# Kernel tuning notes

Hardware: AMD Instinct MI355X
Metric: run time of the kernel (lower is better)

Reference implementation:

```python
import jax, jax.numpy as jnp
import numpy as np

CHUNK = 32  # chunk_size default in delta_rule_chunkwise


def _l2norm(x):
    # matches fla-style l2norm: x / ||x||_2 along last dim
    return x * jax.lax.rsqrt(jnp.sum(x * x, axis=-1, keepdims=True) + 1e-6)


def setup_inputs() -> dict:
    key = jax.random.key(0)
    kq, kk, kv, kb = jax.random.split(key, 4)
    b, h, L, dk, dv = 4, 8, 8192, 64, 64
    q = jax.random.normal(kq, (b, h, L, dk), jnp.float32)
    k = jax.random.normal(kk, (b, h, L, dk), jnp.float32)
    v = jax.random.normal(kv, (b, h, L, dv), jnp.float32)
    beta = jax.random.uniform(kb, (b, h, L), jnp.float32)  # sigmoid(b_proj) in (0,1)
    return {"q": q, "k": k, "v": v, "beta": beta}


def _delta_rule_chunkwise(q, k, v, beta, chunk=CHUNK):
    b, h, L, dk = q.shape
    dv = v.shape[-1]
    assert L % chunk == 0  # L chosen as multiple of chunk -> pad_len == 0
    n = L // chunk

    q = _l2norm(q)
    k = _l2norm(k)
    v = v * beta[..., None]
    k_beta = k * beta[..., None]

    # (b,h,L,d) -> (b,h,n,c,d)
    resh = lambda t: t.reshape(b, h, n, chunk, t.shape[-1])
    qc, kc, vc, kbc = resh(q), resh(k), resh(v), resh(k_beta)

    # intra-chunk triangular inversion: attn = (I - tril(k_beta k^T, -1))^{-1}
    tri = jnp.triu(jnp.ones((chunk, chunk), bool), 0)  # incl. diagonal
    attn = -jnp.einsum('bhnid,bhnjd->bhnij', kbc, kc)
    attn = jnp.where(tri, 0.0, attn)
    for i in range(1, chunk):  # static forward-substitution loop over chunk rows
        row = attn[..., i, :]                                  # (b,h,n,c)
        upd = jnp.einsum('bhnj,bhnjm->bhnm', row, attn)[..., :i]
        attn = attn.at[..., i, :i].add(upd)
    attn = attn + jnp.eye(chunk, dtype=attn.dtype)

    u = attn @ vc   # (b,h,n,c,dv)
    w = attn @ kbc  # (b,h,n,c,dk)

    strict = jnp.triu(jnp.ones((chunk, chunk), bool), 1)

    def step(S, xs):
        q_i, k_i, u_i0, w_i = xs  # (b,h,c,d)
        attn_local = jnp.where(strict, 0.0,
                               jnp.einsum('bhid,bhjd->bhij', q_i, k_i))
        u_i = u_i0 - w_i @ S                       # (b,h,c,dv)
        o_i = q_i @ S + attn_local @ u_i           # (b,h,c,dv)
        S_new = S + jnp.einsum('bhcd,bhcv->bhdv', k_i, u_i)
        return S_new, o_i

    to_scan = lambda t: jnp.moveaxis(t, 2, 0)  # (n,b,h,c,d)
    S0 = jnp.zeros((b, h, dk, dv), q.dtype)
    S, o = jax.lax.scan(step, S0, (to_scan(qc), to_scan(kc), to_scan(u), to_scan(w)))
    o = jnp.moveaxis(o, 0, 2).reshape(b, h, L, dv)
    return o, S


def reference(q, k, v, beta):
    return _delta_rule_chunkwise(q, k, v, beta)
```

## Files before the change

kernel.cpp:

```cpp
#include <hip/hip_runtime.h>

#define CH 32
#define DD 64
#define NCHUNK 256
#define SEQ 8192
#define BH 32
#define NSEG 16
#define CPS 16

typedef _Float16 half8 __attribute__((ext_vector_type(8)));
typedef float f32x4 __attribute__((ext_vector_type(4)));
typedef unsigned short u16;

#define MFMA16(a, b, c) __builtin_amdgcn_mfma_f32_16x16x32_f16((a), (b), (c), 0, 0, 0)

__device__ __forceinline__ void split_store(const float* src8, bool neg, u16* dst) {
    half8 hi, lo;
#pragma unroll
    for (int j = 0; j < 8; ++j) {
        float x = neg ? -src8[j] : src8[j];
        _Float16 xh = (_Float16)x;
        hi[j] = xh;
        lo[j] = (_Float16)(x - (float)xh);
    }
    *(half8*)dst = hi;
    *(half8*)(dst + 8) = lo;
}

__device__ __forceinline__ void hi_store(const float* src8, u16* dst) {
    half8 hi;
#pragma unroll
    for (int j = 0; j < 8; ++j) hi[j] = (_Float16)src8[j];
    *(half8*)dst = hi;
}

__device__ __forceinline__ void split8(const float* src8, half8* hi, half8* lo) {
#pragma unroll
    for (int j = 0; j < 8; ++j) {
        float x = src8[j];
        _Float16 xh = (_Float16)x;
        (*hi)[j] = xh;
        (*lo)[j] = (_Float16)(x - (float)xh);
    }
}

__device__ __forceinline__ void splitB(const f32x4& a, const f32x4& b, half8* hi, half8* lo) {
#pragma unroll
    for (int j = 0; j < 4; ++j) {
        float x = a[j];
        _Float16 xh = (_Float16)x;
        (*hi)[j] = xh; (*lo)[j] = (_Float16)(x - (float)xh);
    }
#pragma unroll
    for (int j = 0; j < 4; ++j) {
        float x = b[j];
        _Float16 xh = (_Float16)x;
        (*hi)[4 + j] = xh; (*lo)[4 + j] = (_Float16)(x - (float)xh);
    }
}

__global__ __launch_bounds__(256) void prep_kernel(
    float* __restrict__ q, float* __restrict__ k,
    const float* __restrict__ v, const float* __restrict__ beta,
    float* __restrict__ u_out, u16* __restrict__ qfrag, u16* __restrict__ pfrag)
{
    const int blk = blockIdx.x;
    const int bh = blk >> 8;
    const int cc = blk & 255;
    const size_t base = ((size_t)bh * SEQ + (size_t)cc * CH) * DD;
    const int t = threadIdx.x;

    __shared__ __align__(16) float qs[CH][68];
    __shared__ __align__(16) float ks[CH][68];
    __shared__ __align__(16) float kb[CH][68];
    __shared__ __align__(16) float vb[CH][68];
    __shared__ __align__(16) float wl[CH][68];
    __shared__ float A[CH][33];
    __shared__ __align__(16) float Pl[CH][36];
    __shared__ float bet[CH];
    __shared__ float rnq[CH];
    __shared__ float rnk[CH];

    if (t < CH) bet[t] = beta[(size_t)bh * SEQ + (size_t)cc * CH + t];
    for (int rep = 0; rep < 2; ++rep) {
        int idx = t + rep * 256;
        int r = idx >> 4, d4 = idx & 15;
        float4 vq = *(const float4*)&q[base + (size_t)idx * 4];
        float4 vk = *(const float4*)&k[base + (size_t)idx * 4];
        float4 vv = *(const float4*)&v[base + (size_t)idx * 4];
        *(float4*)&qs[r][4 * d4] = vq;
        *(float4*)&ks[r][4 * d4] = vk;
        *(float4*)&vb[r][4 * d4] = vv;
    }
    __syncthreads();
    if (t < CH) {
        float ss = 0.f;
        for (int d4 = 0; d4 < 16; ++d4) {
            float4 x = *(const float4*)&qs[t][4 * d4];
            ss += x.x * x.x + x.y * x.y + x.z * x.z + x.w * x.w;
        }
        rnq[t] = rsqrtf(ss + 1e-6f);
    } else if (t < 2 * CH) {
        int r = t - CH;
        float ss = 0.f;
        for (int d4 = 0; d4 < 16; ++d4) {
            float4 x = *(const float4*)&ks[r][4 * d4];
            ss += x.x * x.x + x.y * x.y + x.z * x.z + x.w * x.w;
        }
        rnk[r] = rsqrtf(ss + 1e-6f);
    }
    __syncthreads();
    for (int rep = 0; rep < 2; ++rep) {
        int idx = t + rep * 256;
        int r = idx >> 4, d4 = idx & 15;
        float4 vq = *(const float4*)&qs[r][4 * d4];
        float4 vk = *(const float4*)&ks[r][4 * d4];
        float4 vv = *(const float4*)&vb[r][4 * d4];
        float fq = rnq[r], fk = rnk[r], fb = bet[r];
        vq.x *= fq; vq.y *= fq; vq.z *= fq; vq.w *= fq;
        vk.x *= fk; vk.y *= fk; vk.z *= fk; vk.w *= fk;
        float4 vkb = make_float4(vk.x * fb, vk.y * fb, vk.z * fb, vk.w * fb);
        float4 vvb = make_float4(vv.x * fb, vv.y * fb, vv.z * fb, vv.w * fb);
        *(float4*)&qs[r][4 * d4] = vq;
        *(float4*)&ks[r][4 * d4] = vk;
        *(float4*)&kb[r][4 * d4] = vkb;
        *(float4*)&vb[r][4 * d4] = vvb;
    }
    __syncthreads();
    {
        const int l = t & 63, n = l & 15, h = l >> 4;
        const int wv = t >> 6, mt = wv >> 1, nt = wv & 1;
        half8 kbhi[2], kblo[2], qhi[2], qlo[2], khi[2], klo[2];
#pragma unroll
        for (int kt = 0; kt < 2; ++kt) {
            float a8[8], q8[8], b8[8];
#pragma unroll
            for (int jj = 0; jj < 8; ++jj) {
                a8[jj] = kb[16 * mt + n][32 * kt + 8 * h + jj];
                q8[jj] = qs[16 * mt + n][32 * kt + 8 * h + jj];
                b8[jj] = ks[16 * nt + n][32 * kt + 8 * h + jj];
            }
            split8(a8, &kbhi[kt], &kblo[kt]);
            split8(q8, &qhi[kt], &qlo[kt]);
            split8(b8, &khi[kt], &klo[kt]);
        }
        f32x4 gacc = {0.f, 0.f, 0.f, 0.f};
        f32x4 pacc = {0.f, 0.f, 0.f, 0.f};
#pragma unroll
        for (int kt = 0; kt < 2; ++kt) {
            gacc = MFMA16(kbhi[kt], khi[kt], gacc);
            gacc = MFMA16(kbhi[kt], klo[kt], gacc);
            gacc = MFMA16(kblo[kt], khi[kt], gacc);
            pacc = MFMA16(qhi[kt], khi[kt], pacc);
            pacc = MFMA16(qhi[kt], klo[kt], pacc);
            pacc = MFMA16(qlo[kt], khi[kt], pacc);
        }
#pragma unroll
        for (int i = 0; i < 4; ++i) {
            int ig = 16 * mt + 4 * h + i, jg = 16 * nt + n;
            A[ig][jg] = (jg < ig) ? -gacc[i] : 0.f;
            Pl[ig][jg] = (jg <= ig) ? pacc[i] : 0.f;
        }
    }
    __syncthreads();
    if (t < 64) {
        const int col = t & 31;
        float creg[CH];
        #pragma unroll
        for (int j = 0; j < CH; ++j) creg[j] = A[j][col];
        #pragma unroll
        for (int i = 1; i < CH; ++i) {
            float s = 0.f;
            #pragma unroll
            for (int j = 1; j < i; ++j) s += A[i][j] * creg[j];
            if (col < i) creg[i] += s;
        }
        if (t < 32) {
            #pragma unroll
            for (int j = 0; j < CH; ++j) A[j][col] = creg[j];
        }
    }
    __syncthreads();
    if (t < 128) {
        const int d4 = t & 15;
        const int i0 = (t >> 4) * 4;
        float4 su[4], sw[4];
        #pragma unroll
        for (int ii = 0; ii < 4; ++ii) {
            su[ii] = *(const float4*)&vb[i0 + ii][4 * d4];
            sw[ii] = *(const float4*)&kb[i0 + ii][4 * d4];
        }
        for (int j = 0; j <= i0 + 2; ++j) {
            float4 vv = *(const float4*)&vb[j][4 * d4];
            float4 vk = *(const float4*)&kb[j][4 * d4];
            #pragma unroll
            for (int ii = 0; ii < 4; ++ii) {
                float a = (j < i0 + ii) ? A[i0 + ii][j] : 0.f;
                su[ii].x += a * vv.x; su[ii].y += a * vv.y;
                su[ii].z += a * vv.z; su[ii].w += a * vv.w;
                sw[ii].x += a * vk.x; sw[ii].y += a * vk.y;
                sw[ii].z += a * vk.z; sw[ii].w += a * vk.w;
            }
        }
        #pragma unroll
        for (int ii = 0; ii < 4; ++ii) {
            *(float4*)&u_out[base + (size_t)(i0 + ii) * DD + 4 * d4] = su[ii];
            *(float4*)&wl[i0 + ii][4 * d4] = sw[ii];
        }
    }
    __syncthreads();
    {
        const int l = t & 63;
        const int n = l & 15, h = l >> 4;
        const int tw = t >> 6;
        const int mt = tw >> 1, kt = tw & 1;
        const size_t cslot = (size_t)bh * 256 + cc;
        {
            float tmp[8];
            #pragma unroll
            for (int j = 0; j < 8; ++j) tmp[j] = wl[mt * 16 + n][kt * 32 + h * 8 + j];
            split_store(tmp, true, (u16*)q + cslot * 4096 + (size_t)tw * 1024 + l * 16);
        }
        {
            float tmp[8];
            #pragma unroll
            for (int j = 0; j < 8; ++j) tmp[j] = ks[h * 8 + j][tw * 16 + n];
            split_store(tmp, false, (u16*)k + cslot * 4096 + (size_t)tw * 1024 + l * 16);
        }
        {
            float tmp[8];
            #pragma unroll
            for (int j = 0; j < 8; ++j) tmp[j] = qs[mt * 16 + n][kt * 32 + h * 8 + j];
            hi_store(tmp, qfrag + cslot * 2048 + (size_t)tw * 512 + l * 8);
        }
        if (t < 128) {
            float tmp[8];
            #pragma unroll
            for (int j = 0; j < 8; ++j) tmp[j] = Pl[tw * 16 + n][h * 8 + j];
            hi_store(tmp, pfrag + cslot * 1024 + (size_t)tw * 512 + l * 8);
        }
    }
}

__global__ __launch_bounds__(512) void seg_tf_kernel(
    const u16* __restrict__ wfrag, const u16* __restrict__ ktfrag,
    const float* __restrict__ uo, float* __restrict__ Tbuf, float* __restrict__ Bbuf)
{
    const int bhseg = blockIdx.x;
    const int bh = bhseg >> 4, seg = bhseg & (NSEG - 1);
    const int wv = threadIdx.x >> 6;
    const int g = wv & 3;
    const int tb = wv >> 2;
    const int l = threadIdx.x & 63;
    const int n = l & 15, h = l >> 4;
    const int c0 = seg * CPS, c1 = c0 + CPS;

    __shared__ __align__(16) float Sc[8][16 * 76];
    __shared__ __align__(16) float uc[8][16 * 44];

    const u16* wb = wfrag + (size_t)bh * 256 * 4096;
    const u16* kb = ktfrag + (size_t)bh * 256 * 4096;
    const float* ub = uo + (size_t)bh * SEQ * DD + (size_t)g * 16;

    f32x4 Sacc[4];
    const f32x4 fzero = {0.f, 0.f, 0.f, 0.f};
#pragma unroll
    for (int mt = 0; mt < 4; ++mt) Sacc[mt] = fzero;
    if (!tb) {
#pragma unroll
        for (int mt = 0; mt < 4; ++mt)
#pragma unroll
            for (int i = 0; i < 4; ++i)
                if (16 * mt + 4 * h + i == g * 16 + n) Sacc[mt][i] = 1.f;
    }

    half8 wcur[8];
    float u0cur[8];
#pragma unroll
    for (int z = 0; z < 8; ++z) u0cur[z] = 0.f;
    {
        const u16* wc = wb + (size_t)c0 * 4096;
#pragma unroll
        for (int tw = 0; tw < 4; ++tw) {
            wcur[tw * 2 + 0] = *(const half8*)(wc + (size_t)tw * 1024 + l * 16);
            wcur[tw * 2 + 1] = *(const half8*)(wc + (size_t)tw * 1024 + l * 16 + 8);
        }
        if (tb) {
#pragma unroll
            for (int mt = 0; mt < 2; ++mt)
#pragma unroll
                for (int i = 0; i < 4; ++i)
                    u0cur[mt * 4 + i] = ub[(size_t)(c0 * 32 + mt * 16 + h * 4 + i) * 64 + n];
        }
    }

    for (int c = c0; c < c1; ++c) {
        __syncthreads();
#pragma unroll
        for (int mt = 0; mt < 4; ++mt)
            *(f32x4*)&Sc[wv][n * 76 + mt * 16 + h * 4] = Sacc[mt];

        const u16* kc = kb + (size_t)c * 4096;
        half8 kT[8];
#pragma unroll
        for (int mt = 0; mt < 4; ++mt) {
            kT[mt * 2 + 0] = *(const half8*)(kc + (size_t)mt * 1024 + l * 16);
            kT[mt * 2 + 1] = *(const half8*)(kc + (size_t)mt * 1024 + l * 16 + 8);
        }

        const int cn = (c + 1 < c1) ? c + 1 : c;
        half8 wn[8];
        float u0n[8];
#pragma unroll
        for (int z = 0; z < 8; ++z) u0n[z] = 0.f;
        {
            const u16* wc = wb + (size_t)cn * 4096;
#pragma unroll
            for (int tw = 0; tw < 4; ++tw) {
                wn[tw * 2 + 0] = *(const half8*)(wc + (size_t)tw * 1024 + l * 16);
                wn[tw * 2 + 1] = *(const half8*)(wc + (size_t)tw * 1024 + l * 16 + 8);
            }
            if (tb) {
#pragma unroll
                for (int mt = 0; mt < 2; ++mt)
#pragma unroll
                    for (int i = 0; i < 4; ++i)
                        u0n[mt * 4 + i] = ub[(size_t)(cn * 32 + mt * 16 + h * 4 + i) * 64 + n];
            }
        }

        asm volatile("s_waitcnt lgkmcnt(0)" ::: "memory");
        half8 SBhi[2], SBlo[2];
#pragma unroll
        for (int kt = 0; kt < 2; ++kt) {
            f32x4 a = *(const f32x4*)&Sc[wv][n * 76 + kt * 32 + h * 8];
            f32x4 b = *(const f32x4*)&Sc[wv][n * 76 + kt * 32 + h * 8 + 4];
            splitB(a, b, &SBhi[kt], &SBlo[kt]);
        }

        f32x4 accu[2];
#pragma unroll
        for (int mt = 0; mt < 2; ++mt) {
            f32x4 a;
            a[0] = u0cur[mt * 4 + 0]; a[1] = u0cur[mt * 4 + 1];
            a[2] = u0cur[mt * 4 + 2]; a[3] = u0cur[mt * 4 + 3];
#pragma unroll
            for (int kt = 0; kt < 2; ++kt) {
                const int tw = mt * 2 + kt;
                a = MFMA16(wcur[tw * 2 + 0], SBhi[kt], a);
                a = MFMA16(wcur[tw * 2 + 0], SBlo[kt], a);
                a = MFMA16(wcur[tw * 2 + 1], SBhi[kt], a);
            }
            accu[mt] = a;
        }

#pragma unroll
        for (int mt = 0; mt < 2; ++mt)
            *(f32x4*)&uc[wv][n * 44 + mt * 16 + h * 4] = accu[mt];
        asm volatile("s_waitcnt lgkmcnt(0)" ::: "memory");
        half8 uBhi, uBlo;
        {
            f32x4 a = *(const f32x4*)&uc[wv][n * 44 + h * 8];
            f32x4 b = *(const f32x4*)&uc[wv][n * 44 + h * 8 + 4];
            splitB(a, b, &uBhi, &uBlo);
        }

#pragma unroll
        for (int mt = 0; mt < 4; ++mt) {
            f32x4 a = Sacc[mt];
            a = MFMA16(kT[mt * 2 + 0], uBhi, a);
            a = MFMA16(kT[mt * 2 + 0], uBlo, a);
            a = MFMA16(kT[mt * 2 + 1], uBhi, a);
            Sacc[mt] = a;
        }

#pragma unroll
        for (int z = 0; z < 8; ++z) wcur[z] = wn[z];
#pragma unroll
        for (int z = 0; z < 8; ++z) u0cur[z] = u0n[z];
    }

    float* ob = (tb ? Bbuf : Tbuf) + (size_t)bhseg * 4096;
#pragma unroll
    for (int mt = 0; mt < 4; ++mt)
#pragma unroll
        for (int i = 0; i < 4; ++i)
            ob[(size_t)(16 * mt + 4 * h + i) * 64 + g * 16 + n] = Sacc[mt][i];
}

__global__ __launch_bounds__(64) void compose_kernel(
    const float* __restrict__ Tbuf, const float* __restrict__ Bbuf,
    float* __restrict__ Sst, float* __restrict__ s_out)
{
    const int bh = blockIdx.x & 31;
    const int g = blockIdx.x >> 5;
    const int l = threadIdx.x;
    const int n = l & 15, h = l >> 4;
    __shared__ __align__(16) float Sc[16 * 76];

    f32x4 S[4];
    const f32x4 fzero = {0.f, 0.f, 0.f, 0.f};
#pragma unroll
    for (int mt = 0; mt < 4; ++mt) S[mt] = fzero;

    for (int s = 0; s < NSEG; ++s) {
        const size_t mb = (size_t)(bh * NSEG + s) * 4096;
#pragma unroll
        for (int mt = 0; mt < 4; ++mt)
#pragma unroll
            for (int i = 0; i < 4; ++i)
                Sst[mb + (size_t)(16 * mt + 4 * h + i) * 64 + g * 16 + n] = S[mt][i];

        f32x4 tr[16];
#pragma unroll
        for (int mt = 0; mt < 4; ++mt)
#pragma unroll
            for (int kkt = 0; kkt < 2; ++kkt) {
                tr[mt * 4 + kkt * 2 + 0] =
                    *(const f32x4*)&Tbuf[mb + (size_t)(16 * mt + n) * 64 + 32 * kkt + 8 * h];
                tr[mt * 4 + kkt * 2 + 1] =
                    *(const f32x4*)&Tbuf[mb + (size_t)(16 * mt + n) * 64 + 32 * kkt + 8 * h + 4];
            }
        f32x4 acc[4];
#pragma unroll
        for (int mt = 0; mt < 4; ++mt)
#pragma unroll
            for (int i = 0; i < 4; ++i)
                acc[mt][i] = Bbuf[mb + (size_t)(16 * mt + 4 * h + i) * 64 + g * 16 + n];

#pragma unroll
        for (int mt = 0; mt < 4; ++mt)
            *(f32x4*)&Sc[n * 76 + mt * 16 + h * 4] = S[mt];
        asm volatile("s_waitcnt lgkmcnt(0)" ::: "memory");
        half8 SBhi[2], SBlo[2];
#pragma unroll
        for (int kt = 0; kt < 2; ++kt) {
            f32x4 a = *(const f32x4*)&Sc[n * 76 + kt * 32 + h * 8];
            f32x4 b = *(const f32x4*)&Sc[n * 76 + kt * 32 + h * 8 + 4];
            splitB(a, b, &SBhi[kt], &SBlo[kt]);
        }

#pragma unroll
        for (int mt = 0; mt < 4; ++mt) {
            f32x4 a = acc[mt];
#pragma unroll
            for (int kkt = 0; kkt < 2; ++kkt) {
                float t8[8];
                f32x4 t0 = tr[mt * 4 + kkt * 2 + 0];
                f32x4 t1 = tr[mt * 4 + kkt * 2 + 1];
#pragma unroll
                for (int j = 0; j < 4; ++j) { t8[j] = t0[j]; t8[4 + j] = t1[j]; }
                half8 thi, tlo;
                split8(t8, &thi, &tlo);
                a = MFMA16(thi, SBhi[kkt], a);
                a = MFMA16(thi, SBlo[kkt], a);
                a = MFMA16(tlo, SBhi[kkt], a);
            }
            S[mt] = a;
        }
    }

#pragma unroll
    for (int mt = 0; mt < 4; ++mt)
#pragma unroll
        for (int i = 0; i < 4; ++i)
            s_out[(size_t)bh * (DD * DD) + (size_t)(16 * mt + 4 * h + i) * 64 + g * 16 + n] =
                S[mt][i];
}

__global__ __launch_bounds__(256) void seg_scan_kernel(
    const u16* __restrict__ wfrag, const u16* __restrict__ ktfrag,
    const u16* __restrict__ qfrag, const u16* __restrict__ pfrag,
    const float* __restrict__ Sst, float* __restrict__ uo)
{
    const int bhseg = blockIdx.x;
    const int bh = bhseg >> 4, seg = bhseg & (NSEG - 1);
    const int wv = threadIdx.x >> 6;
    const int g = wv;
    const int l = threadIdx.x & 63;
    const int n = l & 15, h = l >> 4;
    const int c0 = seg * CPS, c1 = c0 + CPS;

    __shared__ __align__(16) float Sc[4][16 * 76];
    __shared__ __align__(16) float uc[4][16 * 44];

    const u16* wb = wfrag + (size_t)bh * 256 * 4096;
    const u16* kb = ktfrag + (size_t)bh * 256 * 4096;
    const u16* qb = qfrag + (size_t)bh * 256 * 2048;
    const u16* pb = pfrag + (size_t)bh * 256 * 1024;
    float* ub = uo + (size_t)bh * SEQ * DD + (size_t)g * 16;

    const f32x4 fzero = {0.f, 0.f, 0.f, 0.f};
    f32x4 Sacc[4];
    {
        const float* sb = Sst + (size_t)bhseg * 4096;
#pragma unroll
        for (int mt = 0; mt < 4; ++mt)
#pragma unroll
            for (int i = 0; i < 4; ++i)
                Sacc[mt][i] = sb[(size_t)(16 * mt + 4 * h + i) * 64 + g * 16 + n];
    }

    half8 wcur[8];
    float u0cur[8];
    {
        const u16* wc = wb + (size_t)c0 * 4096;
#pragma unroll
        for (int tw = 0; tw < 4; ++tw) {
            wcur[tw * 2 + 0] = *(const half8*)(wc + (size_t)tw * 1024 + l * 16);
            wcur[tw * 2 + 1] = *(const half8*)(wc + (size_t)tw * 1024 + l * 16 + 8);
        }
#pragma unroll
        for (int mt = 0; mt < 2; ++mt)
#pragma unroll
            for (int i = 0; i < 4; ++i)
                u0cur[mt * 4 + i] = ub[(size_t)(c0 * 32 + mt * 16 + h * 4 + i) * 64 + n];
    }

    for (int c = c0; c < c1; ++c) {
        __syncthreads();
#pragma unroll
        for (int mt = 0; mt < 4; ++mt)
            *(f32x4*)&Sc[wv][n * 76 + mt * 16 + h * 4] = Sacc[mt];

        const u16* kc = kb + (size_t)c * 4096;
        half8 kT[8];
#pragma unroll
        for (int mt = 0; mt < 4; ++mt) {
            kT[mt * 2 + 0] = *(const half8*)(kc + (size_t)mt * 1024 + l * 16);
            kT[mt * 2 + 1] = *(const half8*)(kc + (size_t)mt * 1024 + l * 16 + 8);
        }
        const u16* qc = qb + (size_t)c * 2048;
        half8 qh[4];
#pragma unroll
        for (int tw = 0; tw < 4; ++tw) qh[tw] = *(const half8*)(qc + (size_t)tw * 512 + l * 8);
        const u16* pc = pb + (size_t)c * 1024;
        half8 Ph[2];
#pragma unroll
        for (int mt = 0; mt < 2; ++mt) Ph[mt] = *(const half8*)(pc + (size_t)mt * 512 + l * 8);

        const int cn = (c + 1 < c1) ? c + 1 : c;
        half8 wn[8];
        float u0n[8];
        {
            const u16* wc = wb + (size_t)cn * 4096;
#pragma unroll
            for (int tw = 0; tw < 4; ++tw) {
                wn[tw * 2 + 0] = *(const half8*)(wc + (size_t)tw * 1024 + l * 16);
                wn[tw * 2 + 1] = *(const half8*)(wc + (size_t)tw * 1024 + l * 16 + 8);
            }
#pragma unroll
            for (int mt = 0; mt < 2; ++mt)
#pragma unroll
                for (int i = 0; i < 4; ++i)
                    u0n[mt * 4 + i] = ub[(size_t)(cn * 32 + mt * 16 + h * 4 + i) * 64 + n];
        }

        asm volatile("s_waitcnt lgkmcnt(0)" ::: "memory");
        half8 SBhi[2], SBlo[2];
#pragma unroll
        for (int kt = 0; kt < 2; ++kt) {
            f32x4 a = *(const f32x4*)&Sc[wv][n * 76 + kt * 32 + h * 8];
            f32x4 b = *(const f32x4*)&Sc[wv][n * 76 + kt * 32 + h * 8 + 4];
            splitB(a, b, &SBhi[kt], &SBlo[kt]);
        }

        f32x4 accu[2];
#pragma unroll
        for (int mt = 0; mt < 2; ++mt) {
            f32x4 a;
            a[0] = u0cur[mt * 4 + 0]; a[1] = u0cur[mt * 4 + 1];
            a[2] = u0cur[mt * 4 + 2]; a[3] = u0cur[mt * 4 + 3];
#pragma unroll
            for (int kt = 0; kt < 2; ++kt) {
                const int tw = mt * 2 + kt;
                a = MFMA16(wcur[tw * 2 + 0], SBhi[kt], a);
                a = MFMA16(wcur[tw * 2 + 0], SBlo[kt], a);
                a = MFMA16(wcur[tw * 2 + 1], SBhi[kt], a);
            }
            accu[mt] = a;
        }

#pragma unroll
        for (int mt = 0; mt < 2; ++mt)
            *(f32x4*)&uc[wv][n * 44 + mt * 16 + h * 4] = accu[mt];
        asm volatile("s_waitcnt lgkmcnt(0)" ::: "memory");
        half8 uBhi, uBlo;
        {
            f32x4 a = *(const f32x4*)&uc[wv][n * 44 + h * 8];
            f32x4 b = *(const f32x4*)&uc[wv][n * 44 + h * 8 + 4];
            splitB(a, b, &uBhi, &uBlo);
        }

#pragma unroll
        for (int mt = 0; mt < 4; ++mt) {
            f32x4 a = Sacc[mt];
            a = MFMA16(kT[mt * 2 + 0], uBhi, a);
            a = MFMA16(kT[mt * 2 + 0], uBlo, a);
            a = MFMA16(kT[mt * 2 + 1], uBhi, a);
            Sacc[mt] = a;
        }

#pragma unroll
        for (int mt = 0; mt < 2; ++mt) {
            f32x4 o = fzero;
#pragma unroll
            for (int kt = 0; kt < 2; ++kt) {
                o = MFMA16(qh[mt * 2 + kt], SBhi[kt], o);
                o = MFMA16(qh[mt * 2 + kt], SBlo[kt], o);
            }
            o = MFMA16(Ph[mt], uBhi, o);
            o = MFMA16(Ph[mt], uBlo, o);
#pragma unroll
            for (int i = 0; i < 4; ++i)
                ub[(size_t)(c * 32 + mt * 16 + h * 4 + i) * 64 + n] = o[i];
        }

#pragma unroll
        for (int z = 0; z < 8; ++z) wcur[z] = wn[z];
#pragma unroll
        for (int z = 0; z < 8; ++z) u0cur[z] = u0n[z];
    }
}

extern "C" void kernel_launch(void* const* d_in, const int* in_sizes, int n_in,
                              void* d_out, int out_size, void* d_ws, size_t ws_size,
                              hipStream_t stream) {
    float* q = (float*)d_in[0];
    float* k = (float*)d_in[1];
    float* v = (float*)d_in[2];
    const float* beta = (const float*)d_in[3];
    float* out = (float*)d_out;
    float* o_region = out;
    float* s_region = out + (size_t)BH * SEQ * DD;
    u16* qfr = (u16*)d_ws;
    u16* pfr = (u16*)((char*)d_ws + 33554432);
    const size_t segfloats = (size_t)BH * NSEG * 4096;
    float* Tbuf = v;
    float* Bbuf = v + segfloats;
    float* Sst = v + 2 * segfloats;

    prep_kernel<<<BH * NCHUNK, 256, 0, stream>>>(q, k, v, beta, o_region, qfr, pfr);
    seg_tf_kernel<<<BH * NSEG, 512, 0, stream>>>((const u16*)q, (const u16*)k,
                                                 o_region, Tbuf, Bbuf);
    compose_kernel<<<128, 64, 0, stream>>>(Tbuf, Bbuf, Sst, s_region);
    seg_scan_kernel<<<BH * NSEG, 256, 0, stream>>>((const u16*)q, (const u16*)k,
                                                   qfr, pfr, Sst, o_region);
}
```

Measured before the change: 441.3 us.

## Fuse segment-state composition into seg_scan and compute l2norm via wave shuffles

The separate compose_kernel is removed. Each seg_scan block now recomputes its own starting state by composing the transfer matrices of all preceding segments, which drops one kernel launch and the serial 16-step dependency carried by only 128 small blocks. The cost is redundant work: later segments redo up to 15 compositions, which adds MFMA and Tbuf/Bbuf reads to the critical path. The prep kernel also computes the q/k row norms with cross-lane xor shuffles instead of shared-memory passes, which removes two __syncthreads and the shared staging.

```diff
diff --git a/kernel.cpp b/kernel.cpp
--- a/kernel.cpp
+++ b/kernel.cpp
@@ -77,46 +77,25 @@
     __shared__ __align__(16) float wl[CH][68];
     __shared__ float A[CH][33];
     __shared__ __align__(16) float Pl[CH][36];
-    __shared__ float bet[CH];
-    __shared__ float rnq[CH];
-    __shared__ float rnk[CH];
-
-    if (t < CH) bet[t] = beta[(size_t)bh * SEQ + (size_t)cc * CH + t];
+
+    const float* betap = beta + (size_t)bh * SEQ + (size_t)cc * CH;
+#pragma unroll
     for (int rep = 0; rep < 2; ++rep) {
         int idx = t + rep * 256;
         int r = idx >> 4, d4 = idx & 15;
         float4 vq = *(const float4*)&q[base + (size_t)idx * 4];
         float4 vk = *(const float4*)&k[base + (size_t)idx * 4];
         float4 vv = *(const float4*)&v[base + (size_t)idx * 4];
-        *(float4*)&qs[r][4 * d4] = vq;
-        *(float4*)&ks[r][4 * d4] = vk;
-        *(float4*)&vb[r][4 * d4] = vv;
-    }
-    __syncthreads();
-    if (t < CH) {
-        float ss = 0.f;
-        for (int d4 = 0; d4 < 16; ++d4) {
-            float4 x = *(const float4*)&qs[t][4 * d4];
-            ss += x.x * x.x + x.y * x.y + x.z * x.z + x.w * x.w;
-        }
-        rnq[t] = rsqrtf(ss + 1e-6f);
-    } else if (t < 2 * CH) {
-        int r = t - CH;
-        float ss = 0.f;
-        for (int d4 = 0; d4 < 16; ++d4) {
-            float4 x = *(const float4*)&ks[r][4 * d4];
-            ss += x.x * x.x + x.y * x.y + x.z * x.z + x.w * x.w;
-        }
-        rnk[r] = rsqrtf(ss + 1e-6f);
-    }
-    __syncthreads();
-    for (int rep = 0; rep < 2; ++rep) {
-        int idx = t + rep * 256;
-        int r = idx >> 4, d4 = idx & 15;
-        float4 vq = *(const float4*)&qs[r][4 * d4];
-        float4 vk = *(const float4*)&ks[r][4 * d4];
-        float4 vv = *(const float4*)&vb[r][4 * d4];
-        float fq = rnq[r], fk = rnk[r], fb = bet[r];
+        float sq = vq.x * vq.x + vq.y * vq.y + vq.z * vq.z + vq.w * vq.w;
+        float sk = vk.x * vk.x + vk.y * vk.y + vk.z * vk.z + vk.w * vk.w;
+#pragma unroll
+        for (int m = 1; m < 16; m <<= 1) {
+            sq += __shfl_xor(sq, m, 64);
+            sk += __shfl_xor(sk, m, 64);
+        }
+        float fq = rsqrtf(sq + 1e-6f);
+        float fk = rsqrtf(sk + 1e-6f);
+        float fb = betap[r];
         vq.x *= fq; vq.y *= fq; vq.z *= fq; vq.w *= fq;
         vk.x *= fk; vk.y *= fk; vk.z *= fk; vk.w *= fk;
         float4 vkb = make_float4(vk.x * fb, vk.y * fb, vk.z * fb, vk.w * fb);
@@ -388,90 +367,11 @@
             ob[(size_t)(16 * mt + 4 * h + i) * 64 + g * 16 + n] = Sacc[mt][i];
 }
 
-__global__ __launch_bounds__(64) void compose_kernel(
-    const float* __restrict__ Tbuf, const float* __restrict__ Bbuf,
-    float* __restrict__ Sst, float* __restrict__ s_out)
-{
-    const int bh = blockIdx.x & 31;
-    const int g = blockIdx.x >> 5;
-    const int l = threadIdx.x;
-    const int n = l & 15, h = l >> 4;
-    __shared__ __align__(16) float Sc[16 * 76];
-
-    f32x4 S[4];
-    const f32x4 fzero = {0.f, 0.f, 0.f, 0.f};
-#pragma unroll
-    for (int mt = 0; mt < 4; ++mt) S[mt] = fzero;
-
-    for (int s = 0; s < NSEG; ++s) {
-        const size_t mb = (size_t)(bh * NSEG + s) * 4096;
-#pragma unroll
-        for (int mt = 0; mt < 4; ++mt)
-#pragma unroll
-            for (int i = 0; i < 4; ++i)
-                Sst[mb + (size_t)(16 * mt + 4 * h + i) * 64 + g * 16 + n] = S[mt][i];
-
-        f32x4 tr[16];
-#pragma unroll
-        for (int mt = 0; mt < 4; ++mt)
-#pragma unroll
-            for (int kkt = 0; kkt < 2; ++kkt) {
-                tr[mt * 4 + kkt * 2 + 0] =
-                    *(const f32x4*)&Tbuf[mb + (size_t)(16 * mt + n) * 64 + 32 * kkt + 8 * h];
-                tr[mt * 4 + kkt * 2 + 1] =
-                    *(const f32x4*)&Tbuf[mb + (size_t)(16 * mt + n) * 64 + 32 * kkt + 8 * h + 4];
-            }
-        f32x4 acc[4];
-#pragma unroll
-        for (int mt = 0; mt < 4; ++mt)
-#pragma unroll
-            for (int i = 0; i < 4; ++i)
-                acc[mt][i] = Bbuf[mb + (size_t)(16 * mt + 4 * h + i) * 64 + g * 16 + n];
-
-#pragma unroll
-        for (int mt = 0; mt < 4; ++mt)
-            *(f32x4*)&Sc[n * 76 + mt * 16 + h * 4] = S[mt];
-        asm volatile("s_waitcnt lgkmcnt(0)" ::: "memory");
-        half8 SBhi[2], SBlo[2];
-#pragma unroll
-        for (int kt = 0; kt < 2; ++kt) {
-            f32x4 a = *(const f32x4*)&Sc[n * 76 + kt * 32 + h * 8];
-            f32x4 b = *(const f32x4*)&Sc[n * 76 + kt * 32 + h * 8 + 4];
-            splitB(a, b, &SBhi[kt], &SBlo[kt]);
-        }
-
-#pragma unroll
-        for (int mt = 0; mt < 4; ++mt) {
-            f32x4 a = acc[mt];
-#pragma unroll
-            for (int kkt = 0; kkt < 2; ++kkt) {
-                float t8[8];
-                f32x4 t0 = tr[mt * 4 + kkt * 2 + 0];
-                f32x4 t1 = tr[mt * 4 + kkt * 2 + 1];
-#pragma unroll
-                for (int j = 0; j < 4; ++j) { t8[j] = t0[j]; t8[4 + j] = t1[j]; }
-                half8 thi, tlo;
-                split8(t8, &thi, &tlo);
-                a = MFMA16(thi, SBhi[kkt], a);
-                a = MFMA16(thi, SBlo[kkt], a);
-                a = MFMA16(tlo, SBhi[kkt], a);
-            }
-            S[mt] = a;
-        }
-    }
-
-#pragma unroll
-    for (int mt = 0; mt < 4; ++mt)
-#pragma unroll
-        for (int i = 0; i < 4; ++i)
-            s_out[(size_t)bh * (DD * DD) + (size_t)(16 * mt + 4 * h + i) * 64 + g * 16 + n] =
-                S[mt][i];
-}
-
 __global__ __launch_bounds__(256) void seg_scan_kernel(
     const u16* __restrict__ wfrag, const u16* __restrict__ ktfrag,
     const u16* __restrict__ qfrag, const u16* __restrict__ pfrag,
-    const float* __restrict__ Sst, float* __restrict__ uo)
+    const float* __restrict__ Tbuf, const float* __restrict__ Bbuf,
+    float* __restrict__ uo, float* __restrict__ s_out)
 {
     const int bhseg = blockIdx.x;
     const int bh = bhseg >> 4, seg = bhseg & (NSEG - 1);
@@ -492,13 +392,67 @@
 
     const f32x4 fzero = {0.f, 0.f, 0.f, 0.f};
     f32x4 Sacc[4];
-    {
-        const float* sb = Sst + (size_t)bhseg * 4096;
-#pragma unroll
-        for (int mt = 0; mt < 4; ++mt)
-#pragma unroll
-            for (int i = 0; i < 4; ++i)
-                Sacc[mt][i] = sb[(size_t)(16 * mt + 4 * h + i) * 64 + g * 16 + n];
+#pragma unroll
+    for (int mt = 0; mt < 4; ++mt) Sacc[mt] = fzero;
+
+    if (seg > 0) {
+        {
+            const size_t mb = (size_t)(bh * NSEG) * 4096;
+#pragma unroll
+            for (int mt = 0; mt < 4; ++mt)
+#pragma unroll
+                for (int i = 0; i < 4; ++i)
+                    Sacc[mt][i] = Bbuf[mb + (size_t)(16 * mt + 4 * h + i) * 64 + g * 16 + n];
+        }
+        for (int s = 1; s < seg; ++s) {
+            const size_t mb = (size_t)(bh * NSEG + s) * 4096;
+            f32x4 tr[16];
+#pragma unroll
+            for (int mt = 0; mt < 4; ++mt)
+#pragma unroll
+                for (int kkt = 0; kkt < 2; ++kkt) {
+                    tr[mt * 4 + kkt * 2 + 0] =
+                        *(const f32x4*)&Tbuf[mb + (size_t)(16 * mt + n) * 64 + 32 * kkt + 8 * h];
+                    tr[mt * 4 + kkt * 2 + 1] =
+                        *(const f32x4*)&Tbuf[mb + (size_t)(16 * mt + n) * 64 + 32 * kkt + 8 * h + 4];
+                }
+            f32x4 acc[4];
+#pragma unroll
+            for (int mt = 0; mt < 4; ++mt)
+#pragma unroll
+                for (int i = 0; i < 4; ++i)
+                    acc[mt][i] = Bbuf[mb + (size_t)(16 * mt + 4 * h + i) * 64 + g * 16 + n];
+
+#pragma unroll
+            for (int mt = 0; mt < 4; ++mt)
+                *(f32x4*)&Sc[wv][n * 76 + mt * 16 + h * 4] = Sacc[mt];
+            asm volatile("s_waitcnt lgkmcnt(0)" ::: "memory");
+            half8 SBhi[2], SBlo[2];
+#pragma unroll
+            for (int kt = 0; kt < 2; ++kt) {
+                f32x4 a = *(const f32x4*)&Sc[wv][n * 76 + kt * 32 + h * 8];
+                f32x4 b = *(const f32x4*)&Sc[wv][n * 76 + kt * 32 + h * 8 + 4];
+                splitB(a, b, &SBhi[kt], &SBlo[kt]);
+            }
+#pragma unroll
+            for (int mt = 0; mt < 4; ++mt) {
+                f32x4 a = acc[mt];
+#pragma unroll
+                for (int kkt = 0; kkt < 2; ++kkt) {
+                    float t8[8];
+                    f32x4 t0 = tr[mt * 4 + kkt * 2 + 0];
+                    f32x4 t1 = tr[mt * 4 + kkt * 2 + 1];
+#pragma unroll
+                    for (int j = 0; j < 4; ++j) { t8[j] = t0[j]; t8[4 + j] = t1[j]; }
+                    half8 thi, tlo;
+                    split8(t8, &thi, &tlo);
+                    a = MFMA16(thi, SBhi[kkt], a);
+                    a = MFMA16(thi, SBlo[kkt], a);
+                    a = MFMA16(tlo, SBhi[kkt], a);
+                }
+                Sacc[mt] = a;
+            }
+        }
     }
 
     half8 wcur[8];
@@ -620,6 +574,15 @@
         for (int z = 0; z < 8; ++z) wcur[z] = wn[z];
 #pragma unroll
         for (int z = 0; z < 8; ++z) u0cur[z] = u0n[z];
+    }
+
+    if (seg == NSEG - 1) {
+#pragma unroll
+        for (int mt = 0; mt < 4; ++mt)
+#pragma unroll
+            for (int i = 0; i < 4; ++i)
+                s_out[(size_t)bh * (DD * DD) + (size_t)(16 * mt + 4 * h + i) * 64 + g * 16 + n] =
+                    Sacc[mt][i];
     }
 }
 
@@ -638,12 +601,11 @@
     const size_t segfloats = (size_t)BH * NSEG * 4096;
     float* Tbuf = v;
     float* Bbuf = v + segfloats;
-    float* Sst = v + 2 * segfloats;
 
     prep_kernel<<<BH * NCHUNK, 256, 0, stream>>>(q, k, v, beta, o_region, qfr, pfr);
     seg_tf_kernel<<<BH * NSEG, 512, 0, stream>>>((const u16*)q, (const u16*)k,
                                                  o_region, Tbuf, Bbuf);
-    compose_kernel<<<128, 64, 0, stream>>>(Tbuf, Bbuf, Sst, s_region);
     seg_scan_kernel<<<BH * NSEG, 256, 0, stream>>>((const u16*)q, (const u16*)k,
-                                                   qfr, pfr, Sst, o_region);
-}
+                                                   qfr, pfr, Tbuf, Bbuf,
+                                                   o_region, s_region);
+}
```

New measurement: 443.1 us. No clear change (+0.4%).
